# Performance work log

Measured on AMD Instinct MI355X. Metric: run time of the kernel, lower is better.

## Reference

```python
import jax, jax.numpy as jnp
import numpy as np

HIGH_T = 0.75
LOW_T = 0.25
EPS = 1e-6


def quantize_four_val(w):
    # {-1, -0.5, 0, 0.5, 1} banding per thresholds (0 band for |w| <= LOW_T)
    return jnp.where(w > HIGH_T, 1.0,
           jnp.where(w > LOW_T, 0.5,
           jnp.where(w < -HIGH_T, -1.0,
           jnp.where(w < -LOW_T, -0.5, 0.0))))


def setup_inputs() -> dict:
    key = jax.random.key(0)
    k1, k2, k3, k4 = jax.random.split(key, 4)
    B, S, D_IN, D_OUT = 4, 2048, 2048, 2048
    x_real = jax.random.normal(k1, (B, S, D_IN), dtype=jnp.float32)
    x_imag = jax.random.normal(k2, (B, S, D_IN), dtype=jnp.float32)
    # unit-normal weights so all four quantization levels are exercised
    weight_re = jax.random.normal(k3, (D_OUT, D_IN), dtype=jnp.float32)
    weight_im = jax.random.normal(k4, (D_OUT, D_IN), dtype=jnp.float32)
    gamma = jnp.ones((2 * D_IN,), dtype=jnp.float32)
    beta = jnp.zeros((2 * D_IN,), dtype=jnp.float32)
    return {"x_real": x_real, "x_imag": x_imag, "weight_re": weight_re,
            "weight_im": weight_im, "gamma": gamma, "beta": beta}


def reference(x_real, x_imag, weight_re, weight_im, gamma, beta):
    d = x_real.shape[-1]
    # LayerNorm over concatenated [real, imag] last dim (2*d)
    x_cat = jnp.concatenate([x_real, x_imag], axis=-1)
    mu = jnp.mean(x_cat, axis=-1, keepdims=True)
    var = jnp.var(x_cat, axis=-1, keepdims=True)
    norm = (x_cat - mu) * jax.lax.rsqrt(var + EPS) * gamma + beta
    nr, ni = norm[..., :d], norm[..., d:]
    # STE: forward uses quantized weights
    qw_re = quantize_four_val(weight_re)
    qw_im = quantize_four_val(weight_im)
    s_re = jnp.mean(jnp.abs(weight_re))
    s_im = jnp.mean(jnp.abs(weight_im))
    y_real = nr @ qw_re.T - ni @ qw_im.T
    y_imag = nr @ qw_im.T + ni @ qw_re.T
    return (y_real * s_re, y_imag * s_im)
```

## Files before the change

kernel.cpp:

```cpp
#include <hip/hip_runtime.h>
#include <hip/hip_bf16.h>

constexpr int D_IN  = 2048;
constexpr int D_OUT = 2048;
constexpr int GM = 4 * 2048;
constexpr int GK = 2 * D_IN;
constexpr int GN = 2 * D_OUT;

typedef __attribute__((ext_vector_type(8))) short bf16x8;
typedef __attribute__((ext_vector_type(4))) float f32x4;

constexpr int QB = 1024;

__device__ inline unsigned short q4bits(float w) {
    if (w >  0.75f) return 0x3F80;
    if (w >  0.25f) return 0x3F00;
    if (w < -0.75f) return 0xBF80;
    if (w < -0.25f) return 0xBF00;
    return 0;
}

__device__ inline unsigned short bf16b(float x) {
    __hip_bfloat16 h = __float2bfloat16(x);
    unsigned short u;
    __builtin_memcpy(&u, &h, 2);
    return u;
}

__global__ __launch_bounds__(256) void quant_kernel(
        const float* __restrict__ wre, const float* __restrict__ wim,
        unsigned short* __restrict__ wq, float* __restrict__ sums) {
    float a = 0.f, b = 0.f;
    int tid = blockIdx.x * 256 + threadIdx.x;
    const float4* wre4 = (const float4*)wre;
    const float4* wim4 = (const float4*)wim;
    for (int c = 0; c < 4; c++) {
        int f4i = tid + c * (QB * 256);
        int idx = f4i * 4;
        int o = idx >> 11;
        int k = idx & (D_IN - 1);
        float4 r = wre4[f4i];
        float4 im = wim4[f4i];
        a += fabsf(r.x) + fabsf(r.y) + fabsf(r.z) + fabsf(r.w);
        b += fabsf(im.x) + fabsf(im.y) + fabsf(im.z) + fabsf(im.w);
        ushort4 qre, qim, nim;
        qre.x = q4bits(r.x);  qre.y = q4bits(r.y);  qre.z = q4bits(r.z);  qre.w = q4bits(r.w);
        qim.x = q4bits(im.x); qim.y = q4bits(im.y); qim.z = q4bits(im.z); qim.w = q4bits(im.w);
        nim.x = qim.x ^ 0x8000; nim.y = qim.y ^ 0x8000;
        nim.z = qim.z ^ 0x8000; nim.w = qim.w ^ 0x8000;
        *(ushort4*)(wq + (size_t)o * GK + k)                  = qre;
        *(ushort4*)(wq + (size_t)o * GK + D_IN + k)           = nim;
        *(ushort4*)(wq + (size_t)(D_OUT + o) * GK + k)        = qim;
        *(ushort4*)(wq + (size_t)(D_OUT + o) * GK + D_IN + k) = qre;
    }
    for (int off = 32; off; off >>= 1) {
        a += __shfl_down(a, off, 64);
        b += __shfl_down(b, off, 64);
    }
    __shared__ float sa[4], sb[4];
    int lane = threadIdx.x & 63, wv = threadIdx.x >> 6;
    if (lane == 0) { sa[wv] = a; sb[wv] = b; }
    __syncthreads();
    if (threadIdx.x == 0) {
        atomicAdd(&sums[0], sa[0] + sa[1] + sa[2] + sa[3]);
        atomicAdd(&sums[1], sb[0] + sb[1] + sb[2] + sb[3]);
    }
}

__global__ __launch_bounds__(256) void ln_kernel(
        const float* __restrict__ xr, const float* __restrict__ xi,
        const float* __restrict__ gamma, const float* __restrict__ beta,
        unsigned short* __restrict__ A) {
    int m = blockIdx.x;
    int t = threadIdx.x;
    const float4* r4 = (const float4*)(xr + (size_t)m * D_IN);
    const float4* i4 = (const float4*)(xi + (size_t)m * D_IN);
    float4 vr[2], vi[2];
    float s = 0.f, ss = 0.f;
    for (int c = 0; c < 2; c++) {
        float4 v = r4[t + c * 256];
        vr[c] = v;
        s  += v.x + v.y + v.z + v.w;
        ss += v.x * v.x + v.y * v.y + v.z * v.z + v.w * v.w;
        v = i4[t + c * 256];
        vi[c] = v;
        s  += v.x + v.y + v.z + v.w;
        ss += v.x * v.x + v.y * v.y + v.z * v.z + v.w * v.w;
    }
    for (int off = 32; off; off >>= 1) {
        s  += __shfl_down(s, off, 64);
        ss += __shfl_down(ss, off, 64);
    }
    __shared__ float red[8];
    __shared__ float smu, srs;
    int lane = t & 63, wv = t >> 6;
    if (lane == 0) { red[wv] = s; red[4 + wv] = ss; }
    __syncthreads();
    if (t == 0) {
        float S  = red[0] + red[1] + red[2] + red[3];
        float SS = red[4] + red[5] + red[6] + red[7];
        float mu  = S * (1.0f / 4096.0f);
        float var = SS * (1.0f / 4096.0f) - mu * mu;
        smu = mu;
        srs = rsqrtf(var + 1e-6f);
    }
    __syncthreads();
    float mu = smu, rs = srs;
    const float4* g4 = (const float4*)gamma;
    const float4* b4 = (const float4*)beta;
    ushort4* Arow = (ushort4*)(A + (size_t)m * GK);
    for (int c = 0; c < 2; c++) {
        int k4 = t + c * 256;
        float4 g = g4[k4], b = b4[k4];
        float4 v = vr[c];
        ushort4 o;
        o.x = bf16b((v.x - mu) * rs * g.x + b.x);
        o.y = bf16b((v.y - mu) * rs * g.y + b.y);
        o.z = bf16b((v.z - mu) * rs * g.z + b.z);
        o.w = bf16b((v.w - mu) * rs * g.w + b.w);
        Arow[k4] = o;
        g = g4[512 + k4]; b = b4[512 + k4];
        v = vi[c];
        o.x = bf16b((v.x - mu) * rs * g.x + b.x);
        o.y = bf16b((v.y - mu) * rs * g.y + b.y);
        o.z = bf16b((v.z - mu) * rs * g.z + b.z);
        o.w = bf16b((v.w - mu) * rs * g.w + b.w);
        Arow[512 + k4] = o;
    }
}

__global__ __launch_bounds__(512, 2) void gemm_kernel(
        const unsigned short* __restrict__ A,
        const unsigned short* __restrict__ Wq,
        const float* __restrict__ sums,
        float* __restrict__ out) {
    constexpr int BM = 256, BN = 256, BK = 64;
    constexpr int NT = GK / BK;
    __shared__ unsigned short shA[2][BM * BK];
    __shared__ unsigned short shB[2][BN * BK];

    int lin = blockIdx.y * gridDim.x + blockIdx.x;
    int swz = (lin & 7) * 64 + (lin >> 3);
    int m0 = (swz >> 4) * BM;
    int n0 = (swz & 15) * BN;

    int t = threadIdx.x;
    int lane = t & 63, wid = t >> 6;
    int wr = wid >> 2, wc = wid & 3;
    int quad = lane >> 4, r = lane & 15;
    int srow = lane >> 3;
    int scol = ((lane & 7) ^ srow) * 8;
    int csw0 = (quad ^ (r & 7)) * 8;

    int aRow0 = (wr * 128 + r) * BK;
    int bRow0 = (wc * 64 + r) * BK;

    f32x4 acc[8][4] = {};
    bf16x8 a[4][2], b[2][2];

#define STAGE(mm, bb, kk, ss) do {                                             \
        int dstRow = wid * 32 + (ss) * 8;                                      \
        const unsigned short* gsrc =                                           \
            ((mm) ? Wq + (size_t)(n0 + dstRow + srow) * GK                     \
                  : A  + (size_t)(m0 + dstRow + srow) * GK)                    \
            + (kk) * BK + scol;                                                \
        unsigned short* lp = ((mm) ? shB[bb] : shA[bb]) + dstRow * BK;         \
        __builtin_amdgcn_global_load_lds(                                      \
            (const __attribute__((address_space(1))) void*)(const void*)gsrc,  \
            (__attribute__((address_space(3))) void*)(void*)lp, 16, 0, 0);     \
    } while (0)

#define READ_A(mh) do {                                                        \
        const short* pa_ = (const short*)shA[cur];                             \
        _Pragma("unroll") for (int im = 0; im < 4; ++im)                       \
        _Pragma("unroll") for (int ks = 0; ks < 2; ++ks)                       \
            a[im][ks] = *(const bf16x8*)(pa_ + aRow0                           \
                + ((mh) * 4 + im) * (16 * BK) + (csw0 ^ (ks * 32)));           \
    } while (0)

#define READ_B(nh) do {                                                        \
        const short* pb_ = (const short*)shB[cur];                             \
        _Pragma("unroll") for (int jn = 0; jn < 2; ++jn)                       \
        _Pragma("unroll") for (int ks = 0; ks < 2; ++ks)                       \
            b[jn][ks] = *(const bf16x8*)(pb_ + bRow0                           \
                + ((nh) * 2 + jn) * (16 * BK) + (csw0 ^ (ks * 32)));           \
    } while (0)

#define MFMA_Q(mh, nh) do {                                                    \
        __builtin_amdgcn_s_setprio(1);                                         \
        _Pragma("unroll") for (int im = 0; im < 4; ++im)                       \
        _Pragma("unroll") for (int jn = 0; jn < 2; ++jn)                       \
        _Pragma("unroll") for (int ks = 0; ks < 2; ++ks)                       \
            acc[(mh) * 4 + im][(nh) * 2 + jn] =                                \
                __builtin_amdgcn_mfma_f32_16x16x32_bf16(                       \
                    a[im][ks], b[jn][ks],                                      \
                    acc[(mh) * 4 + im][(nh) * 2 + jn], 0, 0, 0);               \
        __builtin_amdgcn_s_setprio(0);                                         \
    } while (0)

    #pragma unroll
    for (int ss = 0; ss < 4; ++ss) STAGE(0, 0, 0, ss);
    #pragma unroll
    for (int ss = 0; ss < 4; ++ss) STAGE(1, 0, 0, ss);

    #pragma unroll 2
    for (int kt = 0; kt < NT; ++kt) {
        int cur = kt & 1, nxt = cur ^ 1;
        bool more = (kt < NT - 1);

        __builtin_amdgcn_sched_barrier(0);
        if (more) {
            #pragma unroll
            for (int ss = 0; ss < 4; ++ss) STAGE(0, nxt, kt + 1, ss);
            #pragma unroll
            for (int ss = 0; ss < 4; ++ss) STAGE(1, nxt, kt + 1, ss);
        }
        if (more) asm volatile("s_waitcnt vmcnt(8)" ::: "memory");
        else      asm volatile("s_waitcnt vmcnt(0)" ::: "memory");
        __builtin_amdgcn_s_barrier();
        __builtin_amdgcn_sched_barrier(0);

        READ_A(0); READ_B(0);
        __builtin_amdgcn_s_barrier();
        asm volatile("s_waitcnt lgkmcnt(0)" ::: "memory");
        __builtin_amdgcn_sched_barrier(0);
        MFMA_Q(0, 0);
        __builtin_amdgcn_s_barrier();

        READ_B(1);
        __builtin_amdgcn_s_barrier();
        asm volatile("s_waitcnt lgkmcnt(0)" ::: "memory");
        __builtin_amdgcn_sched_barrier(0);
        MFMA_Q(0, 1);
        __builtin_amdgcn_s_barrier();

        READ_A(1);
        __builtin_amdgcn_s_barrier();
        asm volatile("s_waitcnt lgkmcnt(0)" ::: "memory");
        __builtin_amdgcn_sched_barrier(0);
        MFMA_Q(1, 1);
        __builtin_amdgcn_s_barrier();

        READ_B(0);
        __builtin_amdgcn_s_barrier();
        asm volatile("s_waitcnt lgkmcnt(0)" ::: "memory");
        __builtin_amdgcn_sched_barrier(0);
        MFMA_Q(1, 0);
        __builtin_amdgcn_s_barrier();
    }

#undef STAGE
#undef READ_A
#undef READ_B
#undef MFMA_Q

    float s_re = sums[0] * (1.0f / (2048.0f * 2048.0f));
    float s_im = sums[1] * (1.0f / (2048.0f * 2048.0f));
    float scale;
    float* obase;
    int ncol0;
    if (n0 < D_OUT) { scale = s_re; obase = out;                      ncol0 = n0; }
    else            { scale = s_im; obase = out + (size_t)GM * D_OUT; ncol0 = n0 - D_OUT; }

    #pragma unroll
    for (int f = 0; f < 8; ++f)
        #pragma unroll
        for (int g = 0; g < 4; ++g) {
            int mrow = m0 + wr * 128 + f * 16 + quad * 4;
            int ncol = ncol0 + wc * 64 + g * 16 + r;
            #pragma unroll
            for (int reg = 0; reg < 4; ++reg)
                obase[(size_t)(mrow + reg) * D_OUT + ncol] = acc[f][g][reg] * scale;
        }
}

extern "C" void kernel_launch(void* const* d_in, const int* in_sizes, int n_in,
                              void* d_out, int out_size, void* d_ws, size_t ws_size,
                              hipStream_t stream) {
    const float* xr    = (const float*)d_in[0];
    const float* xi    = (const float*)d_in[1];
    const float* wre   = (const float*)d_in[2];
    const float* wim   = (const float*)d_in[3];
    const float* gamma = (const float*)d_in[4];
    const float* beta  = (const float*)d_in[5];
    float* out = (float*)d_out;

    unsigned short* A  = (unsigned short*)d_ws;
    unsigned short* Wq = (unsigned short*)((char*)d_ws + (size_t)GM * GK * 2);
    float* sums = (float*)((char*)d_ws + (size_t)GM * GK * 2 + (size_t)GN * GK * 2);

    (void)hipMemsetAsync(sums, 0, 2 * sizeof(float), stream);
    quant_kernel<<<QB, 256, 0, stream>>>(wre, wim, Wq, sums);
    ln_kernel<<<GM, 256, 0, stream>>>(xr, xi, gamma, beta, A);
    gemm_kernel<<<dim3(GN / 256, GM / 256), 512, 0, stream>>>(A, Wq, sums, out);
}
```

Measured before the change: 566.0 us.

## Merge prep kernels, drop atomics/memset, deepen GEMM prefetch into finer-grained stages

Merges the LayerNorm and weight-quantization kernels into one launch and replaces the memset plus atomics with per-block partial sums. Each GEMM block reduces those partials itself. The GEMM main loop is restructured to prefetch two K-tiles ahead in half-tile chunks, interleaved with the MFMA phases, and uses two B register sets to cut the LDS reads per iteration. The aim is to remove launch and serialization overhead and to hide global-load latency better. The cost is a redundant partial reduction in every GEMM block and more complex wait-count logic, including an in-place overwrite of the current buffer while it is still being read.

```diff
diff --git a/kernel.cpp b/kernel.cpp
--- a/kernel.cpp
+++ b/kernel.cpp
@@ -27,11 +27,70 @@
     return u;
 }
 
-__global__ __launch_bounds__(256) void quant_kernel(
+__device__ __forceinline__ void ln_unit(int m, int t,
+        const float* __restrict__ xr, const float* __restrict__ xi,
+        const float* __restrict__ gamma, const float* __restrict__ beta,
+        unsigned short* __restrict__ A, float* shf) {
+    const float4* r4 = (const float4*)(xr + (size_t)m * D_IN);
+    const float4* i4 = (const float4*)(xi + (size_t)m * D_IN);
+    float4 vr[2], vi[2];
+    float s = 0.f, ss = 0.f;
+    for (int c = 0; c < 2; c++) {
+        float4 v = r4[t + c * 256];
+        vr[c] = v;
+        s  += v.x + v.y + v.z + v.w;
+        ss += v.x * v.x + v.y * v.y + v.z * v.z + v.w * v.w;
+        v = i4[t + c * 256];
+        vi[c] = v;
+        s  += v.x + v.y + v.z + v.w;
+        ss += v.x * v.x + v.y * v.y + v.z * v.z + v.w * v.w;
+    }
+    for (int off = 32; off; off >>= 1) {
+        s  += __shfl_down(s, off, 64);
+        ss += __shfl_down(ss, off, 64);
+    }
+    int lane = t & 63, wv = t >> 6;
+    if (lane == 0) { shf[wv] = s; shf[4 + wv] = ss; }
+    __syncthreads();
+    if (t == 0) {
+        float S  = shf[0] + shf[1] + shf[2] + shf[3];
+        float SS = shf[4] + shf[5] + shf[6] + shf[7];
+        float mu  = S * (1.0f / 4096.0f);
+        float var = SS * (1.0f / 4096.0f) - mu * mu;
+        shf[8] = mu;
+        shf[9] = rsqrtf(var + 1e-6f);
+    }
+    __syncthreads();
+    float mu = shf[8], rs = shf[9];
+    const float4* g4 = (const float4*)gamma;
+    const float4* b4 = (const float4*)beta;
+    ushort4* Arow = (ushort4*)(A + (size_t)m * GK);
+    for (int c = 0; c < 2; c++) {
+        int k4 = t + c * 256;
+        float4 g = g4[k4], b = b4[k4];
+        float4 v = vr[c];
+        ushort4 o;
+        o.x = bf16b((v.x - mu) * rs * g.x + b.x);
+        o.y = bf16b((v.y - mu) * rs * g.y + b.y);
+        o.z = bf16b((v.z - mu) * rs * g.z + b.z);
+        o.w = bf16b((v.w - mu) * rs * g.w + b.w);
+        Arow[k4] = o;
+        g = g4[512 + k4]; b = b4[512 + k4];
+        v = vi[c];
+        o.x = bf16b((v.x - mu) * rs * g.x + b.x);
+        o.y = bf16b((v.y - mu) * rs * g.y + b.y);
+        o.z = bf16b((v.z - mu) * rs * g.z + b.z);
+        o.w = bf16b((v.w - mu) * rs * g.w + b.w);
+        Arow[512 + k4] = o;
+    }
+}
+
+__device__ __forceinline__ void quant_unit(int qb, int t,
         const float* __restrict__ wre, const float* __restrict__ wim,
-        unsigned short* __restrict__ wq, float* __restrict__ sums) {
+        unsigned short* __restrict__ wq, float* __restrict__ partial,
+        float* shf) {
     float a = 0.f, b = 0.f;
-    int tid = blockIdx.x * 256 + threadIdx.x;
+    int tid = qb * 256 + t;
     const float4* wre4 = (const float4*)wre;
     const float4* wim4 = (const float4*)wim;
     for (int c = 0; c < 4; c++) {
@@ -57,87 +116,39 @@
         a += __shfl_down(a, off, 64);
         b += __shfl_down(b, off, 64);
     }
-    __shared__ float sa[4], sb[4];
-    int lane = threadIdx.x & 63, wv = threadIdx.x >> 6;
-    if (lane == 0) { sa[wv] = a; sb[wv] = b; }
+    int lane = t & 63, wv = t >> 6;
+    if (lane == 0) { shf[wv] = a; shf[4 + wv] = b; }
     __syncthreads();
-    if (threadIdx.x == 0) {
-        atomicAdd(&sums[0], sa[0] + sa[1] + sa[2] + sa[3]);
-        atomicAdd(&sums[1], sb[0] + sb[1] + sb[2] + sb[3]);
-    }
-}
-
-__global__ __launch_bounds__(256) void ln_kernel(
+    if (t == 0) {
+        partial[qb]      = shf[0] + shf[1] + shf[2] + shf[3];
+        partial[QB + qb] = shf[4] + shf[5] + shf[6] + shf[7];
+    }
+}
+
+__global__ __launch_bounds__(256) void prep_kernel(
         const float* __restrict__ xr, const float* __restrict__ xi,
         const float* __restrict__ gamma, const float* __restrict__ beta,
-        unsigned short* __restrict__ A) {
-    int m = blockIdx.x;
-    int t = threadIdx.x;
-    const float4* r4 = (const float4*)(xr + (size_t)m * D_IN);
-    const float4* i4 = (const float4*)(xi + (size_t)m * D_IN);
-    float4 vr[2], vi[2];
-    float s = 0.f, ss = 0.f;
-    for (int c = 0; c < 2; c++) {
-        float4 v = r4[t + c * 256];
-        vr[c] = v;
-        s  += v.x + v.y + v.z + v.w;
-        ss += v.x * v.x + v.y * v.y + v.z * v.z + v.w * v.w;
-        v = i4[t + c * 256];
-        vi[c] = v;
-        s  += v.x + v.y + v.z + v.w;
-        ss += v.x * v.x + v.y * v.y + v.z * v.z + v.w * v.w;
-    }
-    for (int off = 32; off; off >>= 1) {
-        s  += __shfl_down(s, off, 64);
-        ss += __shfl_down(ss, off, 64);
-    }
-    __shared__ float red[8];
-    __shared__ float smu, srs;
-    int lane = t & 63, wv = t >> 6;
-    if (lane == 0) { red[wv] = s; red[4 + wv] = ss; }
-    __syncthreads();
-    if (t == 0) {
-        float S  = red[0] + red[1] + red[2] + red[3];
-        float SS = red[4] + red[5] + red[6] + red[7];
-        float mu  = S * (1.0f / 4096.0f);
-        float var = SS * (1.0f / 4096.0f) - mu * mu;
-        smu = mu;
-        srs = rsqrtf(var + 1e-6f);
-    }
-    __syncthreads();
-    float mu = smu, rs = srs;
-    const float4* g4 = (const float4*)gamma;
-    const float4* b4 = (const float4*)beta;
-    ushort4* Arow = (ushort4*)(A + (size_t)m * GK);
-    for (int c = 0; c < 2; c++) {
-        int k4 = t + c * 256;
-        float4 g = g4[k4], b = b4[k4];
-        float4 v = vr[c];
-        ushort4 o;
-        o.x = bf16b((v.x - mu) * rs * g.x + b.x);
-        o.y = bf16b((v.y - mu) * rs * g.y + b.y);
-        o.z = bf16b((v.z - mu) * rs * g.z + b.z);
-        o.w = bf16b((v.w - mu) * rs * g.w + b.w);
-        Arow[k4] = o;
-        g = g4[512 + k4]; b = b4[512 + k4];
-        v = vi[c];
-        o.x = bf16b((v.x - mu) * rs * g.x + b.x);
-        o.y = bf16b((v.y - mu) * rs * g.y + b.y);
-        o.z = bf16b((v.z - mu) * rs * g.z + b.z);
-        o.w = bf16b((v.w - mu) * rs * g.w + b.w);
-        Arow[512 + k4] = o;
-    }
+        unsigned short* __restrict__ A,
+        const float* __restrict__ wre, const float* __restrict__ wim,
+        unsigned short* __restrict__ wq, float* __restrict__ partial) {
+    __shared__ float shf[10];
+    if (blockIdx.x >= GM) {
+        quant_unit(blockIdx.x - GM, threadIdx.x, wre, wim, wq, partial, shf);
+        return;
+    }
+    ln_unit(blockIdx.x, threadIdx.x, xr, xi, gamma, beta, A, shf);
 }
 
 __global__ __launch_bounds__(512, 2) void gemm_kernel(
         const unsigned short* __restrict__ A,
         const unsigned short* __restrict__ Wq,
-        const float* __restrict__ sums,
+        const float* __restrict__ partial,
         float* __restrict__ out) {
     constexpr int BM = 256, BN = 256, BK = 64;
     constexpr int NT = GK / BK;
     __shared__ unsigned short shA[2][BM * BK];
     __shared__ unsigned short shB[2][BN * BK];
+    __shared__ float shf[10];
 
     int lin = blockIdx.y * gridDim.x + blockIdx.x;
     int swz = (lin & 7) * 64 + (lin >> 3);
@@ -155,112 +166,149 @@
     int aRow0 = (wr * 128 + r) * BK;
     int bRow0 = (wc * 64 + r) * BK;
 
+    {
+        float a = 0.f, b = 0.f;
+        for (int i = t; i < QB; i += 512) { a += partial[i]; b += partial[QB + i]; }
+        for (int off = 32; off; off >>= 1) {
+            a += __shfl_down(a, off, 64);
+            b += __shfl_down(b, off, 64);
+        }
+        if (lane == 0) { shf[wid] = a;  }
+        __syncthreads();
+        if (lane == 0 && wid == 0) {
+        }
+        __syncthreads();
+        if (lane == 0) { shf[wid] = a; }
+        __syncthreads();
+        if (t == 0) {
+            float sa = 0.f; for (int i = 0; i < 8; i++) sa += shf[i];
+            shf[8] = sa * (1.0f / (2048.0f * 2048.0f));
+        }
+        __syncthreads();
+        if (lane == 0) { shf[wid] = b; }
+        __syncthreads();
+        if (t == 0) {
+            float sb = 0.f; for (int i = 0; i < 8; i++) sb += shf[i];
+            shf[9] = sb * (1.0f / (2048.0f * 2048.0f));
+        }
+    }
+
     f32x4 acc[8][4] = {};
-    bf16x8 a[4][2], b[2][2];
-
-#define STAGE(mm, bb, kk, ss) do {                                             \
-        int dstRow = wid * 32 + (ss) * 8;                                      \
-        const unsigned short* gsrc =                                           \
-            ((mm) ? Wq + (size_t)(n0 + dstRow + srow) * GK                     \
-                  : A  + (size_t)(m0 + dstRow + srow) * GK)                    \
-            + (kk) * BK + scol;                                                \
-        unsigned short* lp = ((mm) ? shB[bb] : shA[bb]) + dstRow * BK;         \
-        __builtin_amdgcn_global_load_lds(                                      \
-            (const __attribute__((address_space(1))) void*)(const void*)gsrc,  \
-            (__attribute__((address_space(3))) void*)(void*)lp, 16, 0, 0);     \
-    } while (0)
-
-#define READ_A(mh) do {                                                        \
-        const short* pa_ = (const short*)shA[cur];                             \
+    bf16x8 a[4][2], b0[2][2], b1[2][2];
+
+#define STAGE_A(bb, kk, h) do {                                                \
+        if ((kk) < NT) {                                                       \
+            _Pragma("unroll") for (int ss = 0; ss < 2; ++ss) {                 \
+                int rowBase = (wid >> 2) * 128 + (h) * 64 + (wid & 3) * 16 + ss * 8; \
+                const unsigned short* gp =                                     \
+                    A + (size_t)(m0 + rowBase + srow) * GK + (kk) * BK + scol; \
+                unsigned short* lp = shA[bb] + rowBase * BK;                   \
+                __builtin_amdgcn_global_load_lds(                              \
+                    (const __attribute__((address_space(1))) void*)(const void*)gp, \
+                    (__attribute__((address_space(3))) void*)(void*)lp, 16, 0, 0);  \
+            }                                                                  \
+        }                                                                      \
+    } while (0)
+
+#define STAGE_B(bb, kk, h) do {                                                \
+        if ((kk) < NT) {                                                       \
+            _Pragma("unroll") for (int ss = 0; ss < 2; ++ss) {                 \
+                int rowBase = (wid >> 1) * 64 + (h) * 32 + (wid & 1) * 16 + ss * 8; \
+                const unsigned short* gp =                                     \
+                    Wq + (size_t)(n0 + rowBase + srow) * GK + (kk) * BK + scol;\
+                unsigned short* lp = shB[bb] + rowBase * BK;                   \
+                __builtin_amdgcn_global_load_lds(                              \
+                    (const __attribute__((address_space(1))) void*)(const void*)gp, \
+                    (__attribute__((address_space(3))) void*)(void*)lp, 16, 0, 0);  \
+            }                                                                  \
+        }                                                                      \
+    } while (0)
+
+#define READ_A(bb, mh) do {                                                    \
+        const short* pa_ = (const short*)shA[bb];                              \
         _Pragma("unroll") for (int im = 0; im < 4; ++im)                       \
         _Pragma("unroll") for (int ks = 0; ks < 2; ++ks)                       \
             a[im][ks] = *(const bf16x8*)(pa_ + aRow0                           \
                 + ((mh) * 4 + im) * (16 * BK) + (csw0 ^ (ks * 32)));           \
     } while (0)
 
-#define READ_B(nh) do {                                                        \
-        const short* pb_ = (const short*)shB[cur];                             \
+#define READ_B(bb, nh, dst) do {                                               \
+        const short* pb_ = (const short*)shB[bb];                              \
         _Pragma("unroll") for (int jn = 0; jn < 2; ++jn)                       \
         _Pragma("unroll") for (int ks = 0; ks < 2; ++ks)                       \
-            b[jn][ks] = *(const bf16x8*)(pb_ + bRow0                           \
+            dst[jn][ks] = *(const bf16x8*)(pb_ + bRow0                         \
                 + ((nh) * 2 + jn) * (16 * BK) + (csw0 ^ (ks * 32)));           \
     } while (0)
 
-#define MFMA_Q(mh, nh) do {                                                    \
+#define MFMA_Q(mh, nh, breg) do {                                              \
         __builtin_amdgcn_s_setprio(1);                                         \
         _Pragma("unroll") for (int im = 0; im < 4; ++im)                       \
         _Pragma("unroll") for (int jn = 0; jn < 2; ++jn)                       \
         _Pragma("unroll") for (int ks = 0; ks < 2; ++ks)                       \
             acc[(mh) * 4 + im][(nh) * 2 + jn] =                                \
                 __builtin_amdgcn_mfma_f32_16x16x32_bf16(                       \
-                    a[im][ks], b[jn][ks],                                      \
+                    a[im][ks], breg[jn][ks],                                   \
                     acc[(mh) * 4 + im][(nh) * 2 + jn], 0, 0, 0);               \
         __builtin_amdgcn_s_setprio(0);                                         \
     } while (0)
 
-    #pragma unroll
-    for (int ss = 0; ss < 4; ++ss) STAGE(0, 0, 0, ss);
-    #pragma unroll
-    for (int ss = 0; ss < 4; ++ss) STAGE(1, 0, 0, ss);
-
-    #pragma unroll 2
+#define WAIT_LGKM0 do {                                                        \
+        asm volatile("s_waitcnt lgkmcnt(0)" ::: "memory");                     \
+        __builtin_amdgcn_sched_barrier(0);                                     \
+    } while (0)
+
+    STAGE_A(0, 0, 0); STAGE_B(0, 0, 0); STAGE_B(0, 0, 1); STAGE_A(0, 0, 1);
+    STAGE_A(1, 1, 0); STAGE_B(1, 1, 0); STAGE_B(1, 1, 1);
+    asm volatile("s_waitcnt vmcnt(6)" ::: "memory");
+    __builtin_amdgcn_s_barrier();
+
     for (int kt = 0; kt < NT; ++kt) {
-        int cur = kt & 1, nxt = cur ^ 1;
-        bool more = (kt < NT - 1);
-
+        int cur = kt & 1, nx1 = cur ^ 1;
+
+        READ_A(cur, 0);
+        READ_B(cur, 0, b0);
+        STAGE_A(nx1, kt + 1, 1);
+        asm volatile("s_waitcnt lgkmcnt(8)" ::: "memory");
+        __builtin_amdgcn_s_barrier();
+        WAIT_LGKM0;
+        MFMA_Q(0, 0, b0);
+        __builtin_amdgcn_s_barrier();
+
+        READ_B(cur, 1, b1);
+        STAGE_A(cur, kt + 2, 0);
+        __builtin_amdgcn_s_barrier();
+        WAIT_LGKM0;
+        MFMA_Q(0, 1, b1);
+        __builtin_amdgcn_s_barrier();
+
+        READ_A(cur, 1);
+        STAGE_B(cur, kt + 2, 0);
+        __builtin_amdgcn_s_barrier();
+        WAIT_LGKM0;
+        MFMA_Q(1, 1, b1);
+        __builtin_amdgcn_s_barrier();
+
+        STAGE_B(cur, kt + 2, 1);
+        if (kt < NT - 2) asm volatile("s_waitcnt vmcnt(6)" ::: "memory");
+        else             asm volatile("s_waitcnt vmcnt(0)" ::: "memory");
+        __builtin_amdgcn_s_barrier();
         __builtin_amdgcn_sched_barrier(0);
-        if (more) {
-            #pragma unroll
-            for (int ss = 0; ss < 4; ++ss) STAGE(0, nxt, kt + 1, ss);
-            #pragma unroll
-            for (int ss = 0; ss < 4; ++ss) STAGE(1, nxt, kt + 1, ss);
-        }
-        if (more) asm volatile("s_waitcnt vmcnt(8)" ::: "memory");
-        else      asm volatile("s_waitcnt vmcnt(0)" ::: "memory");
-        __builtin_amdgcn_s_barrier();
-        __builtin_amdgcn_sched_barrier(0);
-
-        READ_A(0); READ_B(0);
-        __builtin_amdgcn_s_barrier();
-        asm volatile("s_waitcnt lgkmcnt(0)" ::: "memory");
-        __builtin_amdgcn_sched_barrier(0);
-        MFMA_Q(0, 0);
-        __builtin_amdgcn_s_barrier();
-
-        READ_B(1);
-        __builtin_amdgcn_s_barrier();
-        asm volatile("s_waitcnt lgkmcnt(0)" ::: "memory");
-        __builtin_amdgcn_sched_barrier(0);
-        MFMA_Q(0, 1);
-        __builtin_amdgcn_s_barrier();
-
-        READ_A(1);
-        __builtin_amdgcn_s_barrier();
-        asm volatile("s_waitcnt lgkmcnt(0)" ::: "memory");
-        __builtin_amdgcn_sched_barrier(0);
-        MFMA_Q(1, 1);
-        __builtin_amdgcn_s_barrier();
-
-        READ_B(0);
-        __builtin_amdgcn_s_barrier();
-        asm volatile("s_waitcnt lgkmcnt(0)" ::: "memory");
-        __builtin_amdgcn_sched_barrier(0);
-        MFMA_Q(1, 0);
-        __builtin_amdgcn_s_barrier();
-    }
-
-#undef STAGE
+        MFMA_Q(1, 0, b0);
+        __builtin_amdgcn_s_barrier();
+    }
+
+#undef STAGE_A
+#undef STAGE_B
 #undef READ_A
 #undef READ_B
 #undef MFMA_Q
-
-    float s_re = sums[0] * (1.0f / (2048.0f * 2048.0f));
-    float s_im = sums[1] * (1.0f / (2048.0f * 2048.0f));
+#undef WAIT_LGKM0
+
     float scale;
     float* obase;
     int ncol0;
-    if (n0 < D_OUT) { scale = s_re; obase = out;                      ncol0 = n0; }
-    else            { scale = s_im; obase = out + (size_t)GM * D_OUT; ncol0 = n0 - D_OUT; }
+    if (n0 < D_OUT) { scale = shf[8]; obase = out;                      ncol0 = n0; }
+    else            { scale = shf[9]; obase = out + (size_t)GM * D_OUT; ncol0 = n0 - D_OUT; }
 
     #pragma unroll
     for (int f = 0; f < 8; ++f)
@@ -287,10 +335,9 @@
 
     unsigned short* A  = (unsigned short*)d_ws;
     unsigned short* Wq = (unsigned short*)((char*)d_ws + (size_t)GM * GK * 2);
-    float* sums = (float*)((char*)d_ws + (size_t)GM * GK * 2 + (size_t)GN * GK * 2);
-
-    (void)hipMemsetAsync(sums, 0, 2 * sizeof(float), stream);
-    quant_kernel<<<QB, 256, 0, stream>>>(wre, wim, Wq, sums);
-    ln_kernel<<<GM, 256, 0, stream>>>(xr, xi, gamma, beta, A);
-    gemm_kernel<<<dim3(GN / 256, GM / 256), 512, 0, stream>>>(A, Wq, sums, out);
-}
+    float* partial = (float*)((char*)d_ws + (size_t)GM * GK * 2 + (size_t)GN * GK * 2);
+
+    prep_kernel<<<GM + QB, 256, 0, stream>>>(xr, xi, gamma, beta, A,
+                                             wre, wim, Wq, partial);
+    gemm_kernel<<<dim3(GN / 256, GM / 256), 512, 0, stream>>>(A, Wq, partial, out);
+}
```

New measurement: 522.6 us. -7.7%, faster.
